# Optimization experiments

Hardware: AMD Instinct MI355X
Metric: run time of the kernel (lower is better)

The kernel has to match this reference:

```python
import jax, jax.numpy as jnp
import numpy as np


def setup_inputs() -> dict:
    key = jax.random.key(0)
    ks = jax.random.split(key, 5)
    B, D, T, H = 32, 256, 1024, 512
    s = 1.0 / np.sqrt(H)  # PyTorch default init scale
    return {
        "x": jax.random.normal(ks[0], (B, D, T), dtype=jnp.float32),
        "W_ih": jax.random.uniform(ks[1], (4 * H, D), jnp.float32, -s, s),
        "W_hh": jax.random.uniform(ks[2], (4 * H, H), jnp.float32, -s, s),
        "b_ih": jax.random.uniform(ks[3], (4 * H,), jnp.float32, -s, s),
        "b_hh": jax.random.uniform(ks[4], (4 * H,), jnp.float32, -s, s),
    }


def reference(x, W_ih, W_hh, b_ih, b_hh):
    # x: [B, in_dim, T] -> permute to [B, T, in_dim] as in the torch module
    B, D, T = x.shape
    H = W_hh.shape[1]
    xt = jnp.transpose(x, (0, 2, 1))  # [B, T, D]
    # Precompute input contribution for all timesteps in one GEMM: [B, T, 4H]
    gx_all = jnp.einsum("btd,gd->btg", xt, W_ih) + b_ih + b_hh
    gx_all = jnp.swapaxes(gx_all, 0, 1)  # [T, B, 4H] for scan

    def step(carry, gx):
        h, c = carry
        g = gx + h @ W_hh.T  # [B, 4H]
        i, f, gg, o = jnp.split(g, 4, axis=-1)  # PyTorch gate order i,f,g,o
        i = jax.nn.sigmoid(i)
        f = jax.nn.sigmoid(f)
        gg = jnp.tanh(gg)
        o = jax.nn.sigmoid(o)
        c = f * c + i * gg
        h = o * jnp.tanh(c)
        return (h, c), h

    h0 = jnp.zeros((B, H), dtype=x.dtype)
    c0 = jnp.zeros((B, H), dtype=x.dtype)
    _, hs = jax.lax.scan(step, (h0, c0), gx_all)  # hs: [T, B, H]
    out = jnp.transpose(hs, (1, 2, 0))  # [B, H, T] (return_sequences=True)
    return out
```

## Files before the change

### kernel.cpp

```cpp
#include <hip/hip_runtime.h>
#include <math.h>


using short8  = __attribute__((ext_vector_type(8))) short;
using f32x4   = __attribute__((ext_vector_type(4))) float;
using float4v = __attribute__((ext_vector_type(4))) float;
using uint4v  = __attribute__((ext_vector_type(4))) unsigned;

__device__ inline unsigned short f2bf(float f) {
    unsigned u = __float_as_uint(f);
    unsigned r = u + 0x7fffu + ((u >> 16) & 1u);
    return (unsigned short)(r >> 16);
}
__device__ inline float fsig(float x) {
    return __builtin_amdgcn_rcpf(1.0f + __expf(-x));
}
__device__ inline float ftanh(float x) {
    return 2.0f * __builtin_amdgcn_rcpf(1.0f + __expf(-2.0f * x)) - 1.0f;
}

__global__ void zero_flags(unsigned* p) {
    p[blockIdx.x * 256 + threadIdx.x] = 0u;
}

__global__ __launch_bounds__(256) void x_transpose(const float* __restrict__ x,
                                                   unsigned short* __restrict__ xT) {
    __shared__ unsigned short tile[64][65];
    const int tid = threadIdx.x;
    const int t0 = blockIdx.x * 64, d0 = blockIdx.y * 64, b = blockIdx.z;
    for (int p = 0; p < 16; p++) {
        int d = p * 4 + (tid >> 6);
        int t = tid & 63;
        tile[d][t] = f2bf(x[(b * 256 + d0 + d) * 1024 + t0 + t]);
    }
    __syncthreads();
    for (int p = 0; p < 16; p++) {
        int t = p * 4 + (tid >> 6);
        int d = tid & 63;
        xT[(size_t)(t0 + t) * 8192 + b * 256 + d0 + d] = tile[d][t];
    }
}

#define GS 33
#define OS 17

__global__ __launch_bounds__(512) void lstm_rec(const unsigned short* __restrict__ xT,
                                                const float* __restrict__ Wih,
                                                const float* __restrict__ Whh,
                                                const float* __restrict__ bih,
                                                const float* __restrict__ bhh,
                                                float* __restrict__ out,
                                                unsigned* flags,
                                                unsigned* hbuf) {
    __shared__ __align__(16) unsigned short h_lds[16 * 512];
    __shared__ __align__(16) unsigned short x_lds[2][16 * 256];
    __shared__ float gates_lds[8 * 16 * GS];
    __shared__ float out_stage[512 * OS];

    const int tid  = threadIdx.x;
    const int wave = tid >> 6;
    const int lane = tid & 63;
    const int quad = lane >> 4, l15 = lane & 15;
    const int l7   = l15 & 7;
    const int group = blockIdx.x & 1;
    const int g     = blockIdx.x >> 1;
    const int gate  = wave >> 1;
    const int kh    = wave & 1;

    short8 whh_frag[2][8];
    short8 wih_frag[2][4];
    float bias_t[2];
    for (int tile = 0; tile < 2; tile++) {
        const int nrow = gate * 512 + g * 32 + tile * 16 + l15;
        for (int ks = 0; ks < 8; ks++) {
            const float* p = &Whh[(size_t)nrow * 512 + kh * 256 + ks * 32 + quad * 8];
            short8 v;
            for (int j = 0; j < 8; j++) v[j] = (short)f2bf(p[j]);
            whh_frag[tile][ks] = v;
        }
        for (int ks = 0; ks < 4; ks++) {
            const float* p = &Wih[(size_t)nrow * 256 + kh * 128 + ks * 32 + quad * 8];
            short8 v;
            for (int j = 0; j < 8; j++) v[j] = (short)f2bf(p[j]);
            wih_frag[tile][ks] = v;
        }
        bias_t[tile] = (kh == 0) ? (bih[nrow] + bhh[nrow]) : 0.0f;
    }

    const int eb = tid >> 5, ek = tid & 31;
    const int e7 = eb & 7;
    const int hidx = g * 32 + ek;

    for (int i = tid; i < 16 * 512; i += 512) h_lds[i] = 0;
    {
        const unsigned short* src = xT + (size_t)(group * 16 + eb) * 256 + ek * 8;
        *(short8*)&x_lds[0][eb * 256 + (ek ^ e7) * 8] = *(const short8*)src;
    }

    float c = 0.0f;
    float* out_base = out + ((size_t)(group * 16 + eb) * 512 + hidx) * 1024;
    unsigned* my_flags = flags + group * 512;
    unsigned* hb_base  = hbuf + group * 8192;

    __syncthreads();

    f32x4 acc0 = f32x4{bias_t[0], bias_t[0], bias_t[0], bias_t[0]};
    f32x4 acc1 = f32x4{bias_t[1], bias_t[1], bias_t[1], bias_t[1]};
    for (int ks = 0; ks < 4; ks++) {
        short8 af = *(const short8*)&x_lds[0][l15 * 256 + (((kh << 4) + (ks << 2) + quad) ^ l7) * 8];
        acc0 = __builtin_amdgcn_mfma_f32_16x16x32_bf16(af, wih_frag[0][ks], acc0, 0, 0, 0);
        acc1 = __builtin_amdgcn_mfma_f32_16x16x32_bf16(af, wih_frag[1][ks], acc1, 0, 0, 0);
    }

    for (int t = 0; t < 1024; t++) {
        for (int ks = 0; ks < 8; ks++) {
            short8 af = *(const short8*)&h_lds[l15 * 512 + (((kh << 5) + (ks << 2) + quad) ^ l7) * 8];
            acc0 = __builtin_amdgcn_mfma_f32_16x16x32_bf16(af, whh_frag[0][ks], acc0, 0, 0, 0);
            acc1 = __builtin_amdgcn_mfma_f32_16x16x32_bf16(af, whh_frag[1][ks], acc1, 0, 0, 0);
        }
        {
            const int prow = (kh * 4 + gate) * 16;
            for (int r = 0; r < 4; r++) {
                gates_lds[(prow + quad * 4 + r) * GS + l15]      = acc0[r];
                gates_lds[(prow + quad * 4 + r) * GS + 16 + l15] = acc1[r];
            }
        }

        if (t + 1 < 1024) {
            const unsigned short* src = xT + (size_t)(t + 1) * 8192 +
                                        (size_t)(group * 16 + eb) * 256 + ek * 8;
            *(short8*)&x_lds[(t + 1) & 1][eb * 256 + (ek ^ e7) * 8] = *(const short8*)src;
        }
        __syncthreads();

        float iv = gates_lds[(0 * 16 + eb) * GS + ek] + gates_lds[(4 * 16 + eb) * GS + ek];
        float fv = gates_lds[(1 * 16 + eb) * GS + ek] + gates_lds[(5 * 16 + eb) * GS + ek];
        float gv = gates_lds[(2 * 16 + eb) * GS + ek] + gates_lds[(6 * 16 + eb) * GS + ek];
        float ov = gates_lds[(3 * 16 + eb) * GS + ek] + gates_lds[(7 * 16 + eb) * GS + ek];
        iv = fsig(iv); fv = fsig(fv); gv = ftanh(gv); ov = fsig(ov);
        c = fv * c + iv * gv;
        float h = ov * ftanh(c);

        out_stage[tid * OS + (t & 15)] = h;

        unsigned my = f2bf(h);
        {
            int phys = (g * 4 + (ek >> 3)) ^ e7;
            h_lds[eb * 512 + phys * 8 + (ek & 7)] = (unsigned short)my;
        }

        unsigned nb = (unsigned)__shfl_xor((int)my, 1);
        if (t < 1023 && !(ek & 1)) {
            __hip_atomic_store(&hb_base[(t & 1) * 4096 + eb * 256 + g * 16 + (ek >> 1)],
                               my | (nb << 16), __ATOMIC_RELAXED, __HIP_MEMORY_SCOPE_AGENT);
        }

        if ((t & 15) == 15) {
            int t0 = t & ~15;
            for (int q = 0; q < 4; q++) {
                float4v v = *(const float4v*)&out_stage[tid * OS + q * 4];
                *(float4v*)&out_base[t0 + q * 4] = v;
            }
        }

        if (t == 1023) break;

        acc0 = f32x4{bias_t[0], bias_t[0], bias_t[0], bias_t[0]};
        acc1 = f32x4{bias_t[1], bias_t[1], bias_t[1], bias_t[1]};
        {
            const unsigned short* xb = x_lds[(t + 1) & 1];
            for (int ks = 0; ks < 4; ks++) {
                short8 af = *(const short8*)&xb[l15 * 256 + (((kh << 4) + (ks << 2) + quad) ^ l7) * 8];
                acc0 = __builtin_amdgcn_mfma_f32_16x16x32_bf16(af, wih_frag[0][ks], acc0, 0, 0, 0);
                acc1 = __builtin_amdgcn_mfma_f32_16x16x32_bf16(af, wih_frag[1][ks], acc1, 0, 0, 0);
            }
        }

        __builtin_amdgcn_s_waitcnt(0);
        __syncthreads();
        if (tid == 0)
            __hip_atomic_store(&my_flags[g * 32], (unsigned)(t + 1),
                               __ATOMIC_RELAXED, __HIP_MEMORY_SCOPE_AGENT);

        if (wave == 0 && lane < 16) {
            while (__hip_atomic_load(&my_flags[lane * 32], __ATOMIC_RELAXED,
                                     __HIP_MEMORY_SCOPE_AGENT) <= (unsigned)t) { }
        }
        __syncthreads();

        if ((ek >> 1) != g) {
            const unsigned long long* src =
                (const unsigned long long*)&hb_base[(t & 1) * 4096 + eb * 256 + ek * 8];
            unsigned long long v0 = __hip_atomic_load(src + 0, __ATOMIC_RELAXED, __HIP_MEMORY_SCOPE_AGENT);
            unsigned long long v1 = __hip_atomic_load(src + 1, __ATOMIC_RELAXED, __HIP_MEMORY_SCOPE_AGENT);
            unsigned long long v2 = __hip_atomic_load(src + 2, __ATOMIC_RELAXED, __HIP_MEMORY_SCOPE_AGENT);
            unsigned long long v3 = __hip_atomic_load(src + 3, __ATOMIC_RELAXED, __HIP_MEMORY_SCOPE_AGENT);
            int pa = (2 * ek) ^ e7;
            int pb = (2 * ek + 1) ^ e7;
            *(uint4v*)&h_lds[eb * 512 + pa * 8] =
                uint4v{(unsigned)v0, (unsigned)(v0 >> 32), (unsigned)v1, (unsigned)(v1 >> 32)};
            *(uint4v*)&h_lds[eb * 512 + pb * 8] =
                uint4v{(unsigned)v2, (unsigned)(v2 >> 32), (unsigned)v3, (unsigned)(v3 >> 32)};
        }
        __syncthreads();
    }
}

extern "C" void kernel_launch(void* const* d_in, const int* in_sizes, int n_in,
                              void* d_out, int out_size, void* d_ws, size_t ws_size,
                              hipStream_t stream) {
    (void)in_sizes; (void)n_in; (void)out_size; (void)ws_size;
    const float* x   = (const float*)d_in[0];
    const float* Wih = (const float*)d_in[1];
    const float* Whh = (const float*)d_in[2];
    const float* bih = (const float*)d_in[3];
    const float* bhh = (const float*)d_in[4];
    float* out = (float*)d_out;

    char* ws = (char*)d_ws;
    unsigned short* xT = (unsigned short*)ws;
    unsigned* flags    = (unsigned*)(ws + 16777216);
    unsigned* hbuf     = (unsigned*)(ws + 16777216 + 8192);

    zero_flags<<<8, 256, 0, stream>>>(flags);
    dim3 gT(16, 4, 32);
    x_transpose<<<gT, 256, 0, stream>>>(x, xT);
    lstm_rec<<<32, 512, 0, stream>>>(xT, Wih, Whh, bih, bhh, out, flags, hbuf);
}
```

Before: 3.140 ms.

## Replace flag-based inter-block barrier with step-tagged h exchange words

Each exchanged h pair is now packed into a 64-bit word carrying the step index. Consumers poll those words directly instead of waiting on a per-block flag plus a block-wide barrier, which removes one global barrier and one flag round trip per timestep. The x input fragments are loaded straight from global memory into registers instead of going through a double-buffered LDS stage, and output flushes move to the start of the next iteration. The cost is doubled hbuf traffic and more polling load traffic. The change also relies on 64-bit atomic stores being observed as single units.

```diff
diff --git a/kernel.cpp b/kernel.cpp
--- a/kernel.cpp
+++ b/kernel.cpp
@@ -19,8 +19,8 @@
     return 2.0f * __builtin_amdgcn_rcpf(1.0f + __expf(-2.0f * x)) - 1.0f;
 }
 
-__global__ void zero_flags(unsigned* p) {
-    p[blockIdx.x * 256 + threadIdx.x] = 0u;
+__global__ void zero_hbuf(unsigned long long* p) {
+    p[blockIdx.x * 256 + threadIdx.x] = 0ull;
 }
 
 __global__ __launch_bounds__(256) void x_transpose(const float* __restrict__ x,
@@ -50,10 +50,8 @@
                                                 const float* __restrict__ bih,
                                                 const float* __restrict__ bhh,
                                                 float* __restrict__ out,
-                                                unsigned* flags,
-                                                unsigned* hbuf) {
+                                                unsigned long long* __restrict__ hbuf) {
     __shared__ __align__(16) unsigned short h_lds[16 * 512];
-    __shared__ __align__(16) unsigned short x_lds[2][16 * 256];
     __shared__ float gates_lds[8 * 16 * GS];
     __shared__ float out_stage[512 * OS];
 
@@ -90,29 +88,47 @@
     const int eb = tid >> 5, ek = tid & 31;
     const int e7 = eb & 7;
     const int hidx = g * 32 + ek;
+    const bool remote = ((ek >> 1) != g);
 
     for (int i = tid; i < 16 * 512; i += 512) h_lds[i] = 0;
-    {
-        const unsigned short* src = xT + (size_t)(group * 16 + eb) * 256 + ek * 8;
-        *(short8*)&x_lds[0][eb * 256 + (ek ^ e7) * 8] = *(const short8*)src;
-    }
+
+    const unsigned short* xbase = xT + (size_t)(group * 16 + l15) * 256 + kh * 128 + quad * 8;
+
+    short8 xf[4];
+#pragma unroll
+    for (int ks = 0; ks < 4; ks++)
+        xf[ks] = *(const short8*)(xbase + (size_t)0 * 8192 + ks * 32);
 
     float c = 0.0f;
     float* out_base = out + ((size_t)(group * 16 + eb) * 512 + hidx) * 1024;
-    unsigned* my_flags = flags + group * 512;
-    unsigned* hb_base  = hbuf + group * 8192;
+    unsigned long long* hb = hbuf + (size_t)group * 8192;
 
     __syncthreads();
 
     f32x4 acc0 = f32x4{bias_t[0], bias_t[0], bias_t[0], bias_t[0]};
     f32x4 acc1 = f32x4{bias_t[1], bias_t[1], bias_t[1], bias_t[1]};
+#pragma unroll
     for (int ks = 0; ks < 4; ks++) {
-        short8 af = *(const short8*)&x_lds[0][l15 * 256 + (((kh << 4) + (ks << 2) + quad) ^ l7) * 8];
-        acc0 = __builtin_amdgcn_mfma_f32_16x16x32_bf16(af, wih_frag[0][ks], acc0, 0, 0, 0);
-        acc1 = __builtin_amdgcn_mfma_f32_16x16x32_bf16(af, wih_frag[1][ks], acc1, 0, 0, 0);
+        acc0 = __builtin_amdgcn_mfma_f32_16x16x32_bf16(xf[ks], wih_frag[0][ks], acc0, 0, 0, 0);
+        acc1 = __builtin_amdgcn_mfma_f32_16x16x32_bf16(xf[ks], wih_frag[1][ks], acc1, 0, 0, 0);
     }
 
     for (int t = 0; t < 1024; t++) {
+        if (t + 1 < 1024) {
+#pragma unroll
+            for (int ks = 0; ks < 4; ks++)
+                xf[ks] = *(const short8*)(xbase + (size_t)(t + 1) * 8192 + ks * 32);
+        }
+        if (t && !(t & 15)) {
+            const int t0 = t - 16;
+#pragma unroll
+            for (int q = 0; q < 4; q++) {
+                float4v v = *(const float4v*)&out_stage[tid * OS + q * 4];
+                *(float4v*)&out_base[t0 + q * 4] = v;
+            }
+        }
+
+#pragma unroll
         for (int ks = 0; ks < 8; ks++) {
             short8 af = *(const short8*)&h_lds[l15 * 512 + (((kh << 5) + (ks << 2) + quad) ^ l7) * 8];
             acc0 = __builtin_amdgcn_mfma_f32_16x16x32_bf16(af, whh_frag[0][ks], acc0, 0, 0, 0);
@@ -120,18 +136,15 @@
         }
         {
             const int prow = (kh * 4 + gate) * 16;
+#pragma unroll
             for (int r = 0; r < 4; r++) {
                 gates_lds[(prow + quad * 4 + r) * GS + l15]      = acc0[r];
                 gates_lds[(prow + quad * 4 + r) * GS + 16 + l15] = acc1[r];
             }
         }
-
-        if (t + 1 < 1024) {
-            const unsigned short* src = xT + (size_t)(t + 1) * 8192 +
-                                        (size_t)(group * 16 + eb) * 256 + ek * 8;
-            *(short8*)&x_lds[(t + 1) & 1][eb * 256 + (ek ^ e7) * 8] = *(const short8*)src;
-        }
-        __syncthreads();
+        asm volatile("s_waitcnt lgkmcnt(0)" ::: "memory");
+        __builtin_amdgcn_s_barrier();
+        asm volatile("" ::: "memory");
 
         float iv = gates_lds[(0 * 16 + eb) * GS + ek] + gates_lds[(4 * 16 + eb) * GS + ek];
         float fv = gates_lds[(1 * 16 + eb) * GS + ek] + gates_lds[(5 * 16 + eb) * GS + ek];
@@ -141,68 +154,67 @@
         c = fv * c + iv * gv;
         float h = ov * ftanh(c);
 
+        unsigned my = f2bf(h);
+        unsigned nb = (unsigned)__shfl_xor((int)my, 1);
+        if (t < 1023 && !(ek & 1)) {
+            __hip_atomic_store(&hb[(t & 1) * 4096 + eb * 256 + g * 16 + (ek >> 1)],
+                               (unsigned long long)(my | (nb << 16)) |
+                                   ((unsigned long long)(unsigned)(t + 1) << 32),
+                               __ATOMIC_RELAXED, __HIP_MEMORY_SCOPE_AGENT);
+        }
+
         out_stage[tid * OS + (t & 15)] = h;
-
-        unsigned my = f2bf(h);
         {
             int phys = (g * 4 + (ek >> 3)) ^ e7;
             h_lds[eb * 512 + phys * 8 + (ek & 7)] = (unsigned short)my;
         }
 
-        unsigned nb = (unsigned)__shfl_xor((int)my, 1);
-        if (t < 1023 && !(ek & 1)) {
-            __hip_atomic_store(&hb_base[(t & 1) * 4096 + eb * 256 + g * 16 + (ek >> 1)],
-                               my | (nb << 16), __ATOMIC_RELAXED, __HIP_MEMORY_SCOPE_AGENT);
-        }
-
-        if ((t & 15) == 15) {
-            int t0 = t & ~15;
-            for (int q = 0; q < 4; q++) {
-                float4v v = *(const float4v*)&out_stage[tid * OS + q * 4];
-                *(float4v*)&out_base[t0 + q * 4] = v;
-            }
-        }
-
         if (t == 1023) break;
+
+        unsigned long long pv[8];
+        unsigned long long* ps = hb + (t & 1) * 4096 + eb * 256 + ek * 8;
+        if (remote) {
+#pragma unroll
+            for (int j = 0; j < 8; j++)
+                pv[j] = __hip_atomic_load(ps + j, __ATOMIC_RELAXED, __HIP_MEMORY_SCOPE_AGENT);
+        }
 
         acc0 = f32x4{bias_t[0], bias_t[0], bias_t[0], bias_t[0]};
         acc1 = f32x4{bias_t[1], bias_t[1], bias_t[1], bias_t[1]};
-        {
-            const unsigned short* xb = x_lds[(t + 1) & 1];
-            for (int ks = 0; ks < 4; ks++) {
-                short8 af = *(const short8*)&xb[l15 * 256 + (((kh << 4) + (ks << 2) + quad) ^ l7) * 8];
-                acc0 = __builtin_amdgcn_mfma_f32_16x16x32_bf16(af, wih_frag[0][ks], acc0, 0, 0, 0);
-                acc1 = __builtin_amdgcn_mfma_f32_16x16x32_bf16(af, wih_frag[1][ks], acc1, 0, 0, 0);
+#pragma unroll
+        for (int ks = 0; ks < 4; ks++) {
+            acc0 = __builtin_amdgcn_mfma_f32_16x16x32_bf16(xf[ks], wih_frag[0][ks], acc0, 0, 0, 0);
+            acc1 = __builtin_amdgcn_mfma_f32_16x16x32_bf16(xf[ks], wih_frag[1][ks], acc1, 0, 0, 0);
+        }
+
+        if (remote) {
+            for (;;) {
+                bool ok = true;
+#pragma unroll
+                for (int j = 0; j < 8; j++)
+                    ok &= ((unsigned)(pv[j] >> 32) > (unsigned)t);
+                if (ok) break;
+#pragma unroll
+                for (int j = 0; j < 8; j++)
+                    pv[j] = __hip_atomic_load(ps + j, __ATOMIC_RELAXED, __HIP_MEMORY_SCOPE_AGENT);
             }
-        }
-
-        __builtin_amdgcn_s_waitcnt(0);
-        __syncthreads();
-        if (tid == 0)
-            __hip_atomic_store(&my_flags[g * 32], (unsigned)(t + 1),
-                               __ATOMIC_RELAXED, __HIP_MEMORY_SCOPE_AGENT);
-
-        if (wave == 0 && lane < 16) {
-            while (__hip_atomic_load(&my_flags[lane * 32], __ATOMIC_RELAXED,
-                                     __HIP_MEMORY_SCOPE_AGENT) <= (unsigned)t) { }
-        }
-        __syncthreads();
-
-        if ((ek >> 1) != g) {
-            const unsigned long long* src =
-                (const unsigned long long*)&hb_base[(t & 1) * 4096 + eb * 256 + ek * 8];
-            unsigned long long v0 = __hip_atomic_load(src + 0, __ATOMIC_RELAXED, __HIP_MEMORY_SCOPE_AGENT);
-            unsigned long long v1 = __hip_atomic_load(src + 1, __ATOMIC_RELAXED, __HIP_MEMORY_SCOPE_AGENT);
-            unsigned long long v2 = __hip_atomic_load(src + 2, __ATOMIC_RELAXED, __HIP_MEMORY_SCOPE_AGENT);
-            unsigned long long v3 = __hip_atomic_load(src + 3, __ATOMIC_RELAXED, __HIP_MEMORY_SCOPE_AGENT);
-            int pa = (2 * ek) ^ e7;
-            int pb = (2 * ek + 1) ^ e7;
+            const int pa = (2 * ek) ^ e7;
+            const int pb = (2 * ek + 1) ^ e7;
             *(uint4v*)&h_lds[eb * 512 + pa * 8] =
-                uint4v{(unsigned)v0, (unsigned)(v0 >> 32), (unsigned)v1, (unsigned)(v1 >> 32)};
+                uint4v{(unsigned)pv[0], (unsigned)pv[1], (unsigned)pv[2], (unsigned)pv[3]};
             *(uint4v*)&h_lds[eb * 512 + pb * 8] =
-                uint4v{(unsigned)v2, (unsigned)(v2 >> 32), (unsigned)v3, (unsigned)(v3 >> 32)};
-        }
-        __syncthreads();
+                uint4v{(unsigned)pv[4], (unsigned)pv[5], (unsigned)pv[6], (unsigned)pv[7]};
+        }
+
+        asm volatile("s_waitcnt lgkmcnt(0)" ::: "memory");
+        __builtin_amdgcn_s_barrier();
+        asm volatile("" ::: "memory");
+    }
+
+#pragma unroll
+    for (int q = 0; q < 4; q++) {
+        float4v v = *(const float4v*)&out_stage[tid * OS + q * 4];
+        *(float4v*)&out_base[1008 + q * 4] = v;
     }
 }
 
@@ -218,12 +230,11 @@
     float* out = (float*)d_out;
 
     char* ws = (char*)d_ws;
-    unsigned short* xT = (unsigned short*)ws;
-    unsigned* flags    = (unsigned*)(ws + 16777216);
-    unsigned* hbuf     = (unsigned*)(ws + 16777216 + 8192);
-
-    zero_flags<<<8, 256, 0, stream>>>(flags);
+    unsigned short* xT       = (unsigned short*)ws;
+    unsigned long long* hbuf = (unsigned long long*)(ws + 16777216);
+
+    zero_hbuf<<<64, 256, 0, stream>>>(hbuf);
     dim3 gT(16, 4, 32);
     x_transpose<<<gT, 256, 0, stream>>>(x, xT);
-    lstm_rec<<<32, 512, 0, stream>>>(xT, Wih, Whh, bih, bhh, out, flags, hbuf);
-}
+    lstm_rec<<<32, 512, 0, stream>>>(xT, Wih, Whh, bih, bhh, out, hbuf);
+}
```

After: 3.939 ms. +25.4%, slower.
